# Optimization experiments

Hardware: AMD Instinct MI355X
Metric: run time of the kernel (lower is better)

## Reference

```python
import jax, jax.numpy as jnp
import numpy as np

N = 100000      # nodes
E = 1600000     # directed edges (avg degree 16)
F_IN = 256      # in_feats
H = 4           # num_heads
D = 32          # n_hidden per head
NEG_SLOPE = 0.2


def setup_inputs() -> dict:
    key = jax.random.key(0)
    k_feat, k_src, k_dst, k_perm, k_w, k_a = jax.random.split(key, 6)
    features = jax.random.normal(k_feat, (N, F_IN), dtype=jnp.float32)
    src = jax.random.randint(k_src, (E,), 0, N, dtype=jnp.int32)
    dst = jax.random.randint(k_dst, (E,), 0, N, dtype=jnp.int32)
    # fixed instance of torch.randperm(N) for the corrupt=True gather
    perm = jax.random.permutation(k_perm, N).astype(jnp.int32)
    W = jax.random.normal(k_w, (F_IN, H * D), dtype=jnp.float32) / np.sqrt(F_IN)
    a = jax.random.normal(k_a, (2, H, D), dtype=jnp.float32) * 0.1
    return dict(features=features, W=W, attn_l=a[0], attn_r=a[1],
                src=src, dst=dst, perm=perm)


def reference(features, W, attn_l, attn_r, src, dst, perm):
    # corrupt=True path: node-permutation gather
    x = features[perm]                                  # [N, F_IN]
    # GAT layer: shared linear projection -> [N, H, D]
    h = (x @ W).reshape(N, H, D)
    # per-node attention half-scores
    el = jnp.sum(h * attn_l, axis=-1)                   # [N, H]
    er = jnp.sum(h * attn_r, axis=-1)                   # [N, H]
    # per-edge raw attention (gather)
    e = jax.nn.leaky_relu(el[src] + er[dst], NEG_SLOPE)  # [E, H]
    # softmax over edges grouped by destination node (segment softmax)
    emax = jax.ops.segment_max(e, dst, num_segments=N)  # [N, H]
    ee = jnp.exp(e - emax[dst])                         # [E, H]
    denom = jax.ops.segment_sum(ee, dst, num_segments=N)  # [N, H]
    alpha = ee / denom[dst]                             # [E, H]
    # weighted neighbor aggregation (gather-scale-scatter)
    msg = h[src] * alpha[:, :, None]                    # [E, H, D]
    out = jax.ops.segment_sum(msg, dst, num_segments=N)  # [N, H, D]
    return jax.nn.elu(out.reshape(N, H * D))            # [N, 128]
```

## Files before the change

kernel.cpp:

```cpp
#include <hip/hip_runtime.h>
#include <hip/hip_bf16.h>
#include <math.h>

#define N_NODES 100000
#define E_EDGES 1600000
#define F_IN    256
#define HD      128
#define NHEAD   4
#define DHEAD   32
#define NEG_SLOPE 0.2f
#define CAP     64
#define NBIN    200
#define BINW    500
#define CHUNK   8192
#define NCHUNK  196
#define BINCAP  16384
#define NC      144
#define NCT     9
#define GEMS1   196
#define GEMS2   195

typedef __attribute__((ext_vector_type(8))) __bf16 bf16x8;
typedef __attribute__((ext_vector_type(4))) float  f32x4;
typedef __attribute__((ext_vector_type(8))) unsigned short u16x8;

__device__ __forceinline__ unsigned short f2bf(float x) {
    unsigned int b = __float_as_uint(x);
    b += 0x7fffu + ((b >> 16) & 1u);
    return (unsigned short)(b >> 16);
}
__device__ __forceinline__ float bf2f(unsigned short u) {
    return __uint_as_float((unsigned int)u << 16);
}

__global__ void k_prep(const float* __restrict__ W, const float* __restrict__ al,
                       const float* __restrict__ ar, unsigned short* __restrict__ wbf,
                       int* __restrict__ cursor) {
    if (blockIdx.x == 0) {
        for (int i = threadIdx.x; i < NBIN; i += NC) cursor[i] = 0;
    }
    const int k = blockIdx.x;
    const int c = threadIdx.x;
    float v;
    if (c < 128) {
        v = W[k * HD + c];
    } else if (c < 132) {
        int h = c - 128; float s = 0.f;
        for (int d = 0; d < DHEAD; d++) s += W[k * HD + h * DHEAD + d] * al[h * DHEAD + d];
        v = s;
    } else if (c < 136) {
        int h = c - 132; float s = 0.f;
        for (int d = 0; d < DHEAD; d++) s += W[k * HD + h * DHEAD + d] * ar[h * DHEAD + d];
        v = s;
    } else {
        v = 0.f;
    }
    *(unsigned short*)((char*)wbf + (size_t)c * 512 + ((2 * k) ^ ((c & 7) << 4))) = f2bf(v);
}

__device__ __forceinline__ void gemm_role(int bid, int tid,
        unsigned char* smem, const float* __restrict__ X,
        const unsigned short* __restrict__ wbf, const int* __restrict__ perm,
        unsigned short* __restrict__ hb, float* __restrict__ el,
        float* __restrict__ er) {
    unsigned short* Bs = (unsigned short*)smem;
    {
        const float4* srcv = (const float4*)wbf;
        float4* dstv = (float4*)Bs;
#pragma unroll
        for (int i = 0; i < 9; i++) dstv[tid + i * 512] = srcv[tid + i * 512];
    }
    __syncthreads();

    const int l   = tid & 63;
    const int wv  = tid >> 6;
    const int l15 = l & 15;
    const int kg  = l >> 4;
    const int rowbase = bid * 256 + wv * 32;

    int r0 = rowbase + l15;      if (r0 >= N_NODES) r0 = N_NODES - 1;
    int r1 = rowbase + 16 + l15; if (r1 >= N_NODES) r1 = N_NODES - 1;
    const float* aptr0 = X + (long)perm[r0] * F_IN + kg * 8;
    const float* aptr1 = X + (long)perm[r1] * F_IN + kg * 8;

    f32x4 acc[2][NCT];
#pragma unroll
    for (int rt = 0; rt < 2; rt++)
#pragma unroll
        for (int ct = 0; ct < NCT; ct++) acc[rt][ct] = (f32x4){0.f, 0.f, 0.f, 0.f};

#pragma unroll
    for (int k0 = 0; k0 < F_IN; k0 += 32) {
        bf16x8 a0, a1;
        {
            float4 v0 = *(const float4*)(aptr0 + k0);
            float4 v1 = *(const float4*)(aptr0 + k0 + 4);
            a0[0]=(__bf16)v0.x; a0[1]=(__bf16)v0.y; a0[2]=(__bf16)v0.z; a0[3]=(__bf16)v0.w;
            a0[4]=(__bf16)v1.x; a0[5]=(__bf16)v1.y; a0[6]=(__bf16)v1.z; a0[7]=(__bf16)v1.w;
        }
        {
            float4 v0 = *(const float4*)(aptr1 + k0);
            float4 v1 = *(const float4*)(aptr1 + k0 + 4);
            a1[0]=(__bf16)v0.x; a1[1]=(__bf16)v0.y; a1[2]=(__bf16)v0.z; a1[3]=(__bf16)v0.w;
            a1[4]=(__bf16)v1.x; a1[5]=(__bf16)v1.y; a1[6]=(__bf16)v1.z; a1[7]=(__bf16)v1.w;
        }
        const int sb = k0 * 2 + kg * 16;
#pragma unroll
        for (int ct = 0; ct < NCT; ct++) {
            int c = ct * 16 + l15;
            bf16x8 b = *(const bf16x8*)((const char*)Bs + c * 512 + (sb ^ ((c & 7) << 4)));
            acc[0][ct] = __builtin_amdgcn_mfma_f32_16x16x32_bf16(a0, b, acc[0][ct], 0, 0, 0);
            acc[1][ct] = __builtin_amdgcn_mfma_f32_16x16x32_bf16(a1, b, acc[1][ct], 0, 0, 0);
        }
    }

#pragma unroll
    for (int rt = 0; rt < 2; rt++)
#pragma unroll
        for (int i = 0; i < 4; i++) {
            int row = rowbase + rt * 16 + kg * 4 + i;
            if (row < N_NODES) {
                unsigned short* op = hb + (long)row * HD + l15;
#pragma unroll
                for (int ct = 0; ct < 8; ct++) op[ct * 16] = f2bf(acc[rt][ct][i]);
                float v = acc[rt][8][i];
                if (l15 < 4)      el[(long)row * 4 + l15]       = v;
                else if (l15 < 8) er[(long)row * 4 + (l15 - 4)] = v;
            }
        }
}

__global__ __launch_bounds__(512, 4) void k_fat1(const float* __restrict__ X,
        const unsigned short* __restrict__ wbf, const int* __restrict__ perm,
        unsigned short* __restrict__ hb, float* __restrict__ el, float* __restrict__ er,
        const int* __restrict__ src, const int* __restrict__ dst,
        int* __restrict__ cursor, unsigned int* __restrict__ binbuf) {
    __shared__ __align__(16) unsigned char smem[73728];
    const int tid = threadIdx.x;

    if (blockIdx.x < NCHUNK) {
        unsigned int*  buf     = (unsigned int*)smem;
        unsigned char* binid   = smem + 32768;
        unsigned int*  hist    = (unsigned int*)(smem + 40960);
        unsigned int*  pfx     = (unsigned int*)(smem + 41792);
        unsigned int*  base_sh = (unsigned int*)(smem + 42624);
        unsigned int*  cnt2    = (unsigned int*)(smem + 43456);
        const int e0 = blockIdx.x * CHUNK;
        const int n = min(CHUNK, E_EDGES - e0);

        for (int i = tid; i < NBIN; i += 512) { hist[i] = 0; cnt2[i] = 0; }
        __syncthreads();
        for (int i = tid; i < n; i += 512) {
            int d = dst[e0 + i];
            atomicAdd(&hist[d / BINW], 1u);
        }
        __syncthreads();
        if (tid < NBIN) pfx[tid] = hist[tid];
        __syncthreads();
        for (int off = 1; off < NBIN; off <<= 1) {
            unsigned v = (tid < NBIN) ? pfx[tid] : 0;
            unsigned u = (tid >= off && tid < NBIN) ? pfx[tid - off] : 0;
            __syncthreads();
            if (tid < NBIN) pfx[tid] = v + u;
            __syncthreads();
        }
        if (tid < NBIN) base_sh[tid] = (unsigned)atomicAdd(cursor + tid, (int)hist[tid]);
        __syncthreads();
        for (int i = tid; i < n; i += 512) {
            int d = dst[e0 + i];
            int s = src[e0 + i];
            int b = d / BINW;
            unsigned pos = atomicAdd(&cnt2[b], 1u);
            unsigned idx = pfx[b] - hist[b] + pos;
            buf[idx] = ((unsigned)(d - b * BINW) << 17) | (unsigned)s;
            binid[idx] = (unsigned char)b;
        }
        __syncthreads();
        for (int i = tid; i < n; i += 512) {
            int b = binid[i];
            unsigned ex = pfx[b] - hist[b];
            unsigned gpos = base_sh[b] + ((unsigned)i - ex);
            if (gpos < BINCAP) binbuf[(long)b * BINCAP + gpos] = buf[i];
        }
    } else {
        gemm_role(blockIdx.x - NCHUNK, tid, smem, X, wbf, perm, hb, el, er);
    }
}

__global__ __launch_bounds__(512, 4) void k_fat2(const unsigned int* __restrict__ binbuf,
        const int* __restrict__ cursor, int* __restrict__ cnt, int* __restrict__ bucket,
        const float* __restrict__ X, const unsigned short* __restrict__ wbf,
        const int* __restrict__ perm, unsigned short* __restrict__ hb,
        float* __restrict__ el, float* __restrict__ er) {
    __shared__ __align__(16) unsigned char smem[73728];
    if (blockIdx.x < NBIN) {
        int* cnt_l = (int*)smem;
        const int b = blockIdx.x;
        const int n = min(cursor[b], BINCAP);
        for (int i = threadIdx.x; i < BINW; i += 512) cnt_l[i] = 0;
        __syncthreads();
        const unsigned int* bp = binbuf + (long)b * BINCAP;
        for (int i = threadIdx.x; i < n; i += 512) {
            unsigned p = bp[i];
            int dl = (int)(p >> 17);
            int s  = (int)(p & 0x1FFFFu);
            int pos = atomicAdd(&cnt_l[dl], 1);
            if (pos < CAP) bucket[((long)b * BINW + dl) * CAP + pos] = s;
        }
        __syncthreads();
        for (int i = threadIdx.x; i < BINW; i += 512) cnt[b * BINW + i] = cnt_l[i];
    } else {
        gemm_role(GEMS1 + (blockIdx.x - NBIN), threadIdx.x, smem, X, wbf, perm,
                  hb, el, er);
    }
}

__global__ __launch_bounds__(256) void k_aggr(const float* __restrict__ el,
        const float* __restrict__ er, const int* __restrict__ cnt,
        const int* __restrict__ bucket, const unsigned short* __restrict__ hb,
        float* __restrict__ out) {
    int wid = (int)((blockIdx.x * (long)blockDim.x + threadIdx.x) >> 6);
    if (wid >= N_NODES) return;
    const int lane = threadIdx.x & 63;
    const int g    = lane >> 4;
    const int l4   = lane & 15;
    const int head = l4 >> 2;
    int deg = cnt[wid];
    if (deg > CAP) deg = CAP;
    const float ern = er[(long)wid * 4 + head];
    int myS = (lane < deg) ? bucket[(long)wid * CAP + lane] : 0;
    float acc[8];
#pragma unroll
    for (int j = 0; j < 8; j++) acc[j] = 0.f;
    float asum = 0.f;
    for (int i = 0; i < deg; i += 4) {
        int e = i + g;
        int s = __shfl(myS, e & 63, 64);
        u16x8 hv = *(const u16x8*)(hb + (long)s * HD + l4 * 8);
        float a = 0.f;
        if (e < deg) {
            float v = el[(long)s * 4 + head] + ern;
            v = v > 0.f ? v : NEG_SLOPE * v;
            a = __expf(v);
        }
        asum += a;
#pragma unroll
        for (int j = 0; j < 8; j++) acc[j] += bf2f(hv[j]) * a;
    }
#pragma unroll
    for (int off = 16; off <= 32; off <<= 1) {
        asum += __shfl_xor(asum, off, 64);
#pragma unroll
        for (int j = 0; j < 8; j++) acc[j] += __shfl_xor(acc[j], off, 64);
    }
    if (g == 0) {
        float inv = asum > 0.f ? 1.f / asum : 0.f;
        float4 o0, o1;
        float t;
        t = acc[0] * inv; o0.x = t > 0.f ? t : __expf(t) - 1.f;
        t = acc[1] * inv; o0.y = t > 0.f ? t : __expf(t) - 1.f;
        t = acc[2] * inv; o0.z = t > 0.f ? t : __expf(t) - 1.f;
        t = acc[3] * inv; o0.w = t > 0.f ? t : __expf(t) - 1.f;
        t = acc[4] * inv; o1.x = t > 0.f ? t : __expf(t) - 1.f;
        t = acc[5] * inv; o1.y = t > 0.f ? t : __expf(t) - 1.f;
        t = acc[6] * inv; o1.z = t > 0.f ? t : __expf(t) - 1.f;
        t = acc[7] * inv; o1.w = t > 0.f ? t : __expf(t) - 1.f;
        float* op = out + (long)wid * HD + l4 * 8;
        *(float4*)op = o0;
        *(float4*)(op + 4) = o1;
    }
}

extern "C" void kernel_launch(void* const* d_in, const int* in_sizes, int n_in,
                              void* d_out, int out_size, void* d_ws, size_t ws_size,
                              hipStream_t stream) {
    const float* features = (const float*)d_in[0];
    const float* W        = (const float*)d_in[1];
    const float* attn_l   = (const float*)d_in[2];
    const float* attn_r   = (const float*)d_in[3];
    const int*   src      = (const int*)d_in[4];
    const int*   dst      = (const int*)d_in[5];
    const int*   perm     = (const int*)d_in[6];
    float* out = (float*)d_out;

    char* ws = (char*)d_ws;
    const size_t OFF_HB   = 0;
    const size_t OFF_EL   = 25600000;
    const size_t OFF_ER   = 27200000;
    const size_t OFF_CNT  = 28800000;
    const size_t OFF_CUR  = 29200000;
    const size_t OFF_WBF  = 29204096;
    const size_t OFF_BKT  = 29286016;
    const size_t OFF_BINB = 54886016;

    unsigned short* hb    = (unsigned short*)(ws + OFF_HB);
    float* el     = (float*)(ws + OFF_EL);
    float* er     = (float*)(ws + OFF_ER);
    int*   cnt    = (int*)(ws + OFF_CNT);
    int*   cursor = (int*)(ws + OFF_CUR);
    unsigned short* wbf = (unsigned short*)(ws + OFF_WBF);
    int*   bucket = (int*)(ws + OFF_BKT);
    unsigned int* binbuf = (unsigned int*)(ws + OFF_BINB);

    k_prep<<<F_IN, NC, 0, stream>>>(W, attn_l, attn_r, wbf, cursor);
    k_fat1<<<NCHUNK + GEMS1, 512, 0, stream>>>(features, wbf, perm, hb, el, er,
                                               src, dst, cursor, binbuf);
    k_fat2<<<NBIN + GEMS2, 512, 0, stream>>>(binbuf, cursor, cnt, bucket,
                                             features, wbf, perm, hb, el, er);
    k_aggr<<<(N_NODES * 64 + 255) / 256, 256, 0, stream>>>(el, er, cnt, bucket, hb, out);
}
```

Baseline: 134.4 us.

## Replace fixed-capacity per-node buckets with compact CSR edge list

The second binning pass now counts edges per destination in shared memory, runs a block prefix scan, and computes a global bin base from the per-bin cursors, so source indices are written into a compact CSR array instead of padded 64-slot buckets. The aggregation kernel reads each node's neighbours from a per-node base offset. This shrinks the bucket storage and makes neighbour reads contiguous. The cost is a second pass over the bin data, a serial-step scan with many barriers, and one extra base lookup per node.

```diff
diff --git a/kernel.cpp b/kernel.cpp
--- a/kernel.cpp
+++ b/kernel.cpp
@@ -9,7 +9,6 @@
 #define NHEAD   4
 #define DHEAD   32
 #define NEG_SLOPE 0.2f
-#define CAP     64
 #define NBIN    200
 #define BINW    500
 #define CHUNK   8192
@@ -188,37 +187,69 @@
 }
 
 __global__ __launch_bounds__(512, 4) void k_fat2(const unsigned int* __restrict__ binbuf,
-        const int* __restrict__ cursor, int* __restrict__ cnt, int* __restrict__ bucket,
+        const int* __restrict__ cursor, int* __restrict__ cnt, int* __restrict__ basearr,
+        int* __restrict__ csr,
         const float* __restrict__ X, const unsigned short* __restrict__ wbf,
         const int* __restrict__ perm, unsigned short* __restrict__ hb,
         float* __restrict__ el, float* __restrict__ er) {
     __shared__ __align__(16) unsigned char smem[73728];
+    const int tid = threadIdx.x;
     if (blockIdx.x < NBIN) {
         int* cnt_l = (int*)smem;
+        int* pfx_l = (int*)(smem + 2048);
+        int* pos_l = (int*)(smem + 4096);
+        int* redsh = (int*)(smem + 6144);
         const int b = blockIdx.x;
         const int n = min(cursor[b], BINCAP);
-        for (int i = threadIdx.x; i < BINW; i += 512) cnt_l[i] = 0;
-        __syncthreads();
+
+        int part = (tid < b) ? min(cursor[tid], BINCAP) : 0;
+#pragma unroll
+        for (int off = 32; off; off >>= 1) part += __shfl_xor(part, off, 64);
+        if ((tid & 63) == 0) redsh[tid >> 6] = part;
+        for (int i = tid; i < BINW; i += 512) { cnt_l[i] = 0; pos_l[i] = 0; }
+        __syncthreads();
+        if (tid == 0) {
+            int s = 0;
+            for (int i = 0; i < 8; i++) s += redsh[i];
+            redsh[8] = s;
+        }
+        __syncthreads();
+        const int binbase = redsh[8];
+
         const unsigned int* bp = binbuf + (long)b * BINCAP;
-        for (int i = threadIdx.x; i < n; i += 512) {
+        for (int i = tid; i < n; i += 512) atomicAdd(&cnt_l[bp[i] >> 17], 1);
+        __syncthreads();
+        if (tid < BINW) pfx_l[tid] = cnt_l[tid];
+        __syncthreads();
+        for (int off = 1; off < BINW; off <<= 1) {
+            int v = (tid < BINW) ? pfx_l[tid] : 0;
+            int u = (tid >= off && tid < BINW) ? pfx_l[tid - off] : 0;
+            __syncthreads();
+            if (tid < BINW) pfx_l[tid] = v + u;
+            __syncthreads();
+        }
+        for (int i = tid; i < n; i += 512) {
             unsigned p = bp[i];
             int dl = (int)(p >> 17);
             int s  = (int)(p & 0x1FFFFu);
-            int pos = atomicAdd(&cnt_l[dl], 1);
-            if (pos < CAP) bucket[((long)b * BINW + dl) * CAP + pos] = s;
-        }
-        __syncthreads();
-        for (int i = threadIdx.x; i < BINW; i += 512) cnt[b * BINW + i] = cnt_l[i];
+            int pos = atomicAdd(&pos_l[dl], 1);
+            csr[binbase + (pfx_l[dl] - cnt_l[dl]) + pos] = s;
+        }
+        __syncthreads();
+        for (int i = tid; i < BINW; i += 512) {
+            int gd = b * BINW + i;
+            cnt[gd]     = cnt_l[i];
+            basearr[gd] = binbase + pfx_l[i] - cnt_l[i];
+        }
     } else {
-        gemm_role(GEMS1 + (blockIdx.x - NBIN), threadIdx.x, smem, X, wbf, perm,
-                  hb, el, er);
+        gemm_role(GEMS1 + (blockIdx.x - NBIN), tid, smem, X, wbf, perm, hb, el, er);
     }
 }
 
 __global__ __launch_bounds__(256) void k_aggr(const float* __restrict__ el,
         const float* __restrict__ er, const int* __restrict__ cnt,
-        const int* __restrict__ bucket, const unsigned short* __restrict__ hb,
-        float* __restrict__ out) {
+        const int* __restrict__ basearr, const int* __restrict__ csr,
+        const unsigned short* __restrict__ hb, float* __restrict__ out) {
     int wid = (int)((blockIdx.x * (long)blockDim.x + threadIdx.x) >> 6);
     if (wid >= N_NODES) return;
     const int lane = threadIdx.x & 63;
@@ -226,9 +257,10 @@
     const int l4   = lane & 15;
     const int head = l4 >> 2;
     int deg = cnt[wid];
-    if (deg > CAP) deg = CAP;
+    if (deg > 64) deg = 64;
+    const int base = basearr[wid];
     const float ern = er[(long)wid * 4 + head];
-    int myS = (lane < deg) ? bucket[(long)wid * CAP + lane] : 0;
+    int myS = (lane < deg) ? csr[base + lane] : 0;
     float acc[8];
 #pragma unroll
     for (int j = 0; j < 8; j++) acc[j] = 0.f;
@@ -288,24 +320,27 @@
     const size_t OFF_EL   = 25600000;
     const size_t OFF_ER   = 27200000;
     const size_t OFF_CNT  = 28800000;
-    const size_t OFF_CUR  = 29200000;
-    const size_t OFF_WBF  = 29204096;
-    const size_t OFF_BKT  = 29286016;
-    const size_t OFF_BINB = 54886016;
+    const size_t OFF_BASE = 29200000;
+    const size_t OFF_CUR  = 29600000;
+    const size_t OFF_WBF  = 29604096;
+    const size_t OFF_CSR  = 29686016;
+    const size_t OFF_BINB = 36086016;
 
     unsigned short* hb    = (unsigned short*)(ws + OFF_HB);
     float* el     = (float*)(ws + OFF_EL);
     float* er     = (float*)(ws + OFF_ER);
     int*   cnt    = (int*)(ws + OFF_CNT);
+    int*   basearr= (int*)(ws + OFF_BASE);
     int*   cursor = (int*)(ws + OFF_CUR);
     unsigned short* wbf = (unsigned short*)(ws + OFF_WBF);
-    int*   bucket = (int*)(ws + OFF_BKT);
+    int*   csr    = (int*)(ws + OFF_CSR);
     unsigned int* binbuf = (unsigned int*)(ws + OFF_BINB);
 
     k_prep<<<F_IN, NC, 0, stream>>>(W, attn_l, attn_r, wbf, cursor);
     k_fat1<<<NCHUNK + GEMS1, 512, 0, stream>>>(features, wbf, perm, hb, el, er,
                                                src, dst, cursor, binbuf);
-    k_fat2<<<NBIN + GEMS2, 512, 0, stream>>>(binbuf, cursor, cnt, bucket,
+    k_fat2<<<NBIN + GEMS2, 512, 0, stream>>>(binbuf, cursor, cnt, basearr, csr,
                                              features, wbf, perm, hb, el, er);
-    k_aggr<<<(N_NODES * 64 + 255) / 256, 256, 0, stream>>>(el, er, cnt, bucket, hb, out);
-}
+    k_aggr<<<(N_NODES * 64 + 255) / 256, 256, 0, stream>>>(el, er, cnt, basearr, csr,
+                                                           hb, out);
+}
```

After: 130.4 us. 1.03x faster.
